# Kernel tuning notes

Hardware: AMD Instinct MI355X
Metric: run time of the kernel (lower is better)

## Reference

```python
import jax, jax.numpy as jnp
import numpy as np

N_NODES = 50000
N_EDGES = 800000
HIDDEN = 128


def setup_inputs() -> dict:
    key = jax.random.key(0)
    k1, k2, k3, k4, k5 = jax.random.split(key, 5)
    x = jax.random.normal(k1, (N_NODES, HIDDEN), dtype=jnp.float32)
    src = jax.random.randint(k2, (N_EDGES,), 0, N_NODES, dtype=jnp.int32)
    # guarantee every node has in-degree >= 1 so deg**-0.5 is finite
    dst = jnp.concatenate([
        jnp.arange(N_NODES, dtype=jnp.int32),
        jax.random.randint(k3, (N_EDGES - N_NODES,), 0, N_NODES, dtype=jnp.int32),
    ])
    edge_index = jnp.stack([src, dst], axis=0)  # [2, E] (row0=j/src, row1=i/dst)
    # nn.Linear(hidden, hidden) params (reused twice in the original module)
    lim = 1.0 / np.sqrt(HIDDEN)
    W = jax.random.uniform(k4, (HIDDEN, HIDDEN), jnp.float32, -lim, lim)
    b = jax.random.uniform(k5, (HIDDEN,), jnp.float32, -lim, lim)
    return {"x": x, "W": W, "b": b, "edge_index": edge_index}


def reference(x, W, b, edge_index):
    src, dst = edge_index[0], edge_index[1]  # (j, i)
    n = x.shape[0]
    # in-degree via scatter-add
    deg = jnp.zeros((n,), x.dtype).at[dst].add(jnp.ones_like(dst, x.dtype))
    deg_inv_sqrt = deg ** -0.5
    norm = deg_inv_sqrt[src] * deg_inv_sqrt[dst]  # [E]
    # first linear (same weights used twice in original)
    h = x @ W.T + b  # [N, H]
    # COO SpMM: gather source rows, scale, scatter-add to destinations
    msg = h[src] * norm[:, None]  # [E, H]
    agg = jax.ops.segment_sum(msg, dst, num_segments=n)  # [N, H]
    # second linear + exact-erf GELU (torch default); dropout is identity in eval
    out = jax.nn.gelu(agg @ W.T + b, approximate=False)
    return out
```

## Files before the change

### kernel.cpp

```cpp
#include <hip/hip_runtime.h>
#include <hip/hip_bf16.h>

#define HIDDEN 128
#define CAP 64
#define BCAP 8192
#define CHUNK 1024

typedef __attribute__((ext_vector_type(8))) short bf16x8;
typedef __attribute__((ext_vector_type(4))) float f32x4;

__device__ __forceinline__ unsigned short f2bf(float f) {
    unsigned int u = __float_as_uint(f);
    u += 0x7FFFu + ((u >> 16) & 1u);
    return (unsigned short)(u >> 16);
}

__device__ __forceinline__ float bflo(unsigned int u) { return __uint_as_float(u << 16); }
__device__ __forceinline__ float bfhi(unsigned int u) { return __uint_as_float(u & 0xffff0000u); }

__global__ void prep_kernel(const float* __restrict__ x, const float* __restrict__ W,
                            unsigned short* __restrict__ xb, unsigned short* __restrict__ wb,
                            int nx4, int nw4, int partBlocks,
                            const int* __restrict__ ei, int E,
                            unsigned int* __restrict__ cursor,
                            unsigned int* __restrict__ lists,
                            int N) {
    __shared__ unsigned int hist[256], basea[256], cur[256];
    if ((int)blockIdx.x >= partBlocks) {
        int i = (blockIdx.x - partBlocks) * blockDim.x + threadIdx.x;
        if (i < nx4) {
            float4 v = ((const float4*)x)[i];
            ushort4 o;
            o.x = f2bf(v.x); o.y = f2bf(v.y); o.z = f2bf(v.z); o.w = f2bf(v.w);
            ((ushort4*)xb)[i] = o;
        } else {
            int j = i - nx4;
            if (j < nw4) {
                float4 v = ((const float4*)W)[j];
                ushort4 o;
                o.x = f2bf(v.x); o.y = f2bf(v.y); o.z = f2bf(v.z); o.w = f2bf(v.w);
                ((ushort4*)wb)[j] = o;
            }
        }
        return;
    }
    int e0 = blockIdx.x * CHUNK;
    int e1 = e0 + CHUNK; if (e1 > E) e1 = E;
    int tid = threadIdx.x;
    hist[tid] = 0;
    __syncthreads();
    for (int e = e0 + tid; e < e1; e += 256)
        atomicAdd(&hist[ei[E + e] >> 8], 1u);
    __syncthreads();
    unsigned int h = hist[tid];
    basea[tid] = h ? atomicAdd(&cursor[tid], h) : 0u;
    cur[tid] = 0;
    __syncthreads();
    for (int e = e0 + tid; e < e1; e += 256) {
        int s = ei[e];
        int d = ei[E + e];
        int bk = d >> 8;
        unsigned int pos = atomicAdd(&cur[bk], 1u) + basea[bk];
        if (pos < BCAP)
            lists[(size_t)bk * BCAP + pos] = ((unsigned int)s << 8) | (unsigned int)(d & 255);
    }
}

__global__ void buildcsr_kernel(const unsigned int* __restrict__ cursor,
                                const unsigned int* __restrict__ lists,
                                unsigned short* __restrict__ csr,
                                unsigned char* __restrict__ cnt_out,
                                float* __restrict__ dinv, int N) {
    __shared__ unsigned int lcnt[256];
    __shared__ unsigned short lcsr[256 * CAP];
    int b = blockIdx.x;
    int tid = threadIdx.x;
    lcnt[tid] = 0;
    __syncthreads();
    int count = (int)cursor[b]; if (count > BCAP) count = BCAP;
    for (int i = tid; i < count; i += 256) {
        unsigned int pk = lists[(size_t)b * BCAP + i];
        int local = pk & 255;
        unsigned int slot = atomicAdd(&lcnt[local], 1u);
        if (slot < CAP) lcsr[local * CAP + slot] = (unsigned short)(pk >> 8);
    }
    __syncthreads();
    int node = b * 256 + tid;
    if (node < N) {
        unsigned int deg = lcnt[tid];
        cnt_out[node] = (unsigned char)(deg > CAP ? CAP : deg);
        dinv[node] = deg ? rsqrtf((float)deg) : 0.0f;
    }
    const unsigned int* s32 = (const unsigned int*)lcsr;
    unsigned int* d32 = (unsigned int*)(csr + (size_t)b * 256 * CAP);
#pragma unroll
    for (int i = 0; i < 256 * CAP / 2 / 256; i++)
        d32[tid + i * 256] = s32[tid + i * 256];
}

__global__ void agg_kernel(const unsigned char* __restrict__ cnt,
                           const unsigned short* __restrict__ csr,
                           const float* __restrict__ dinv,
                           const unsigned short* __restrict__ xb,
                           unsigned short* __restrict__ yb, float* __restrict__ cvec, int n) {
    int lane = threadIdx.x & 63;
    int wid  = threadIdx.x >> 6;
    int gl   = lane & 15;
    int node = blockIdx.x * 16 + wid * 4 + (lane >> 4);
    if (node >= n) return;

    int deg = cnt[node];
    float di = dinv[node];
    const unsigned short* seg = csr + (size_t)node * CAP;

    float acc0 = 0, acc1 = 0, acc2 = 0, acc3 = 0, acc4 = 0, acc5 = 0, acc6 = 0, acc7 = 0;
    float fs = 0.0f;

    for (int be = 0; be < deg; be += 16) {
        int m = deg - be; if (m > 16) m = 16;
        int sv = (gl < m) ? (int)seg[be + gl] : 0;
        float dvv = (gl < m) ? dinv[sv] : 0.0f;
        for (int e = 0; e < m; e++) {
            int s = __shfl(sv, e, 16);
            float f = __shfl(dvv, e, 16) * di;
            fs += f;
            uint4 hv = *(const uint4*)(xb + (size_t)s * HIDDEN + gl * 8);
            acc0 += f * bflo(hv.x); acc1 += f * bfhi(hv.x);
            acc2 += f * bflo(hv.y); acc3 += f * bfhi(hv.y);
            acc4 += f * bflo(hv.z); acc5 += f * bfhi(hv.z);
            acc6 += f * bflo(hv.w); acc7 += f * bfhi(hv.w);
        }
    }

    uint4 o;
    o.x = (unsigned int)f2bf(acc0) | ((unsigned int)f2bf(acc1) << 16);
    o.y = (unsigned int)f2bf(acc2) | ((unsigned int)f2bf(acc3) << 16);
    o.z = (unsigned int)f2bf(acc4) | ((unsigned int)f2bf(acc5) << 16);
    o.w = (unsigned int)f2bf(acc6) | ((unsigned int)f2bf(acc7) << 16);
    *(uint4*)(yb + (size_t)node * HIDDEN + gl * 8) = o;
    if (gl == 0) cvec[node] = fs;
}

__global__ void dgemm_kernel(const unsigned short* __restrict__ yb,
                             const unsigned short* __restrict__ wb,
                             const float* __restrict__ bias,
                             const float* __restrict__ cvec,
                             float* __restrict__ out, int nrows) {
    __shared__ unsigned short wlds[HIDDEN * HIDDEN];
    __shared__ unsigned short zs[4][16][136];
    int lane = threadIdx.x & 63;
    int wave = threadIdx.x >> 6;
    int base = blockIdx.x * 64 + wave * 16;
    int hi = lane >> 4, lo = lane & 15;

    for (int ci = threadIdx.x; ci < 1024; ci += 256) {
        int r = ci >> 3, c32 = ci & 7;
        const uint4* src = (const uint4*)(wb + (size_t)r * HIDDEN + c32 * 16);
        uint4 v0 = src[0], v1 = src[1];
        int b0 = r * 256 + c32 * 32;
        int sw = (r & 7) << 4;
        *(uint4*)((char*)wlds + (b0 ^ sw)) = v0;
        *(uint4*)((char*)wlds + ((b0 + 16) ^ sw)) = v1;
    }

    int arow = base + lo;
    if (arow >= nrows) arow = nrows - 1;
    const bf16x8* Ap = (const bf16x8*)(yb + (size_t)arow * HIDDEN + hi * 8);
    bf16x8 a0 = Ap[0], a1 = Ap[4], a2 = Ap[8], a3 = Ap[12];
    __syncthreads();

#define BFRAG(T, KK) \
    (*(const bf16x8*)((const char*)wlds + \
        ((((T) * 16 + lo) * 256 + (KK) * 64 + hi * 16) ^ ((lo & 7) << 4))))

    f32x4 acc[8];
#pragma unroll
    for (int t = 0; t < 8; t++) acc[t] = (f32x4)(0.0f);
#pragma unroll
    for (int t = 0; t < 8; t++) {
        acc[t] = __builtin_amdgcn_mfma_f32_16x16x32_bf16(a0, BFRAG(t, 0), acc[t], 0, 0, 0);
        acc[t] = __builtin_amdgcn_mfma_f32_16x16x32_bf16(a1, BFRAG(t, 1), acc[t], 0, 0, 0);
        acc[t] = __builtin_amdgcn_mfma_f32_16x16x32_bf16(a2, BFRAG(t, 2), acc[t], 0, 0, 0);
        acc[t] = __builtin_amdgcn_mfma_f32_16x16x32_bf16(a3, BFRAG(t, 3), acc[t], 0, 0, 0);
    }

    float cv[4];
#pragma unroll
    for (int i = 0; i < 4; i++) {
        int r = base + hi * 4 + i;
        cv[i] = cvec[r < nrows ? r : nrows - 1];
    }
#pragma unroll
    for (int t = 0; t < 8; t++) {
        float bv = bias[t * 16 + lo];
#pragma unroll
        for (int i = 0; i < 4; i++)
            zs[wave][hi * 4 + i][t * 16 + lo] = f2bf(acc[t][i] + cv[i] * bv);
    }

    bf16x8 z0 = *(const bf16x8*)&zs[wave][lo][0 * 32 + hi * 8];
    bf16x8 z1 = *(const bf16x8*)&zs[wave][lo][1 * 32 + hi * 8];
    bf16x8 z2 = *(const bf16x8*)&zs[wave][lo][2 * 32 + hi * 8];
    bf16x8 z3 = *(const bf16x8*)&zs[wave][lo][3 * 32 + hi * 8];

    f32x4 acc2[8];
#pragma unroll
    for (int t = 0; t < 8; t++) acc2[t] = (f32x4)(0.0f);
#pragma unroll
    for (int t = 0; t < 8; t++) {
        acc2[t] = __builtin_amdgcn_mfma_f32_16x16x32_bf16(z0, BFRAG(t, 0), acc2[t], 0, 0, 0);
        acc2[t] = __builtin_amdgcn_mfma_f32_16x16x32_bf16(z1, BFRAG(t, 1), acc2[t], 0, 0, 0);
        acc2[t] = __builtin_amdgcn_mfma_f32_16x16x32_bf16(z2, BFRAG(t, 2), acc2[t], 0, 0, 0);
        acc2[t] = __builtin_amdgcn_mfma_f32_16x16x32_bf16(z3, BFRAG(t, 3), acc2[t], 0, 0, 0);
    }
#undef BFRAG

#pragma unroll
    for (int t = 0; t < 8; t++) {
        int col = t * 16 + lo;
        float bv = bias[col];
#pragma unroll
        for (int i = 0; i < 4; i++) {
            int r = base + hi * 4 + i;
            if (r < nrows) {
                float v = acc2[t][i] + bv;
                v = 0.5f * v * (1.0f + erff(v * 0.70710678118f));
                out[(size_t)r * HIDDEN + col] = v;
            }
        }
    }
}

extern "C" void kernel_launch(void* const* d_in, const int* in_sizes, int n_in,
                              void* d_out, int out_size, void* d_ws, size_t ws_size,
                              hipStream_t stream) {
    const float* x  = (const float*)d_in[0];
    const float* W  = (const float*)d_in[1];
    const float* b  = (const float*)d_in[2];
    const int*   ei = (const int*)d_in[3];

    int N = in_sizes[0] / HIDDEN;
    int E = in_sizes[3] / 2;
    int NB = (N + 255) >> 8;

    char* ws = (char*)d_ws;
    size_t off = 0;
    unsigned int* cursor = (unsigned int*)(ws + off);    off += 1024;
    unsigned int* lists = (unsigned int*)(ws + off);     off += (((size_t)NB * BCAP * 4) + 255) & ~255ull;
    unsigned short* csr = (unsigned short*)(ws + off);   off += (((size_t)NB * 256 * CAP * 2) + 255) & ~255ull;
    unsigned char* cnt = (unsigned char*)(ws + off);     off += (((size_t)N) + 255) & ~255ull;
    float* dinv = (float*)(ws + off);                    off += (((size_t)N * 4) + 255) & ~255ull;
    unsigned short* xb = (unsigned short*)(ws + off);    off += (((size_t)N * HIDDEN * 2) + 255) & ~255ull;
    unsigned short* wb = (unsigned short*)(ws + off);    off += ((HIDDEN * HIDDEN * 2) + 255) & ~255ull;
    unsigned short* yb = (unsigned short*)(ws + off);    off += (((size_t)N * HIDDEN * 2) + 255) & ~255ull;
    float* cvec = (float*)(ws + off);                    off += (((size_t)N * 4) + 255) & ~255ull;

    hipMemsetAsync(cursor, 0, 1024, stream);

    int nx4 = N * HIDDEN / 4, nw4 = HIDDEN * HIDDEN / 4;
    int convBlocks = (nx4 + nw4 + 255) / 256;
    int partBlocks = (E + CHUNK - 1) / CHUNK;
    prep_kernel<<<partBlocks + convBlocks, 256, 0, stream>>>(
        x, W, xb, wb, nx4, nw4, partBlocks, ei, E, cursor, lists, N);
    buildcsr_kernel<<<NB, 256, 0, stream>>>(cursor, lists, csr, cnt, dinv, N);
    agg_kernel<<<(N + 15) / 16, 256, 0, stream>>>(cnt, csr, dinv, xb, yb, cvec, N);
    dgemm_kernel<<<(N + 63) / 64, 256, 0, stream>>>(yb, wb, b, cvec, (float*)d_out, N);
}
```

Baseline: 167.8 us.

## Fuse sparse aggregation into the dense double-GEMM kernel via LDS staging

Merges the gather-based aggregation kernel into the MFMA GEMM kernel. Each wave now aggregates its own 16 rows, four nodes at a time, into shared memory, then feeds them straight into the two chained matmuls. This removes the global write and re-read of the intermediate bf16 matrix and the cvec array, plus one kernel launch. In exchange each block does more serial work before the MFMA phase, and the grid is 4x smaller (64 nodes per block instead of 16), which may reduce latency hiding for the irregular gathers. The 32KB of weights in LDS also limits occupancy for the gather phase.

```diff
diff --git a/kernel.cpp b/kernel.cpp
--- a/kernel.cpp
+++ b/kernel.cpp
@@ -98,56 +98,16 @@
         d32[tid + i * 256] = s32[tid + i * 256];
 }
 
-__global__ void agg_kernel(const unsigned char* __restrict__ cnt,
-                           const unsigned short* __restrict__ csr,
-                           const float* __restrict__ dinv,
-                           const unsigned short* __restrict__ xb,
-                           unsigned short* __restrict__ yb, float* __restrict__ cvec, int n) {
-    int lane = threadIdx.x & 63;
-    int wid  = threadIdx.x >> 6;
-    int gl   = lane & 15;
-    int node = blockIdx.x * 16 + wid * 4 + (lane >> 4);
-    if (node >= n) return;
-
-    int deg = cnt[node];
-    float di = dinv[node];
-    const unsigned short* seg = csr + (size_t)node * CAP;
-
-    float acc0 = 0, acc1 = 0, acc2 = 0, acc3 = 0, acc4 = 0, acc5 = 0, acc6 = 0, acc7 = 0;
-    float fs = 0.0f;
-
-    for (int be = 0; be < deg; be += 16) {
-        int m = deg - be; if (m > 16) m = 16;
-        int sv = (gl < m) ? (int)seg[be + gl] : 0;
-        float dvv = (gl < m) ? dinv[sv] : 0.0f;
-        for (int e = 0; e < m; e++) {
-            int s = __shfl(sv, e, 16);
-            float f = __shfl(dvv, e, 16) * di;
-            fs += f;
-            uint4 hv = *(const uint4*)(xb + (size_t)s * HIDDEN + gl * 8);
-            acc0 += f * bflo(hv.x); acc1 += f * bfhi(hv.x);
-            acc2 += f * bflo(hv.y); acc3 += f * bfhi(hv.y);
-            acc4 += f * bflo(hv.z); acc5 += f * bfhi(hv.z);
-            acc6 += f * bflo(hv.w); acc7 += f * bfhi(hv.w);
-        }
-    }
-
-    uint4 o;
-    o.x = (unsigned int)f2bf(acc0) | ((unsigned int)f2bf(acc1) << 16);
-    o.y = (unsigned int)f2bf(acc2) | ((unsigned int)f2bf(acc3) << 16);
-    o.z = (unsigned int)f2bf(acc4) | ((unsigned int)f2bf(acc5) << 16);
-    o.w = (unsigned int)f2bf(acc6) | ((unsigned int)f2bf(acc7) << 16);
-    *(uint4*)(yb + (size_t)node * HIDDEN + gl * 8) = o;
-    if (gl == 0) cvec[node] = fs;
-}
-
-__global__ void dgemm_kernel(const unsigned short* __restrict__ yb,
-                             const unsigned short* __restrict__ wb,
-                             const float* __restrict__ bias,
-                             const float* __restrict__ cvec,
-                             float* __restrict__ out, int nrows) {
+__global__ void aggdgemm_kernel(const unsigned char* __restrict__ cnt,
+                                const unsigned short* __restrict__ csr,
+                                const float* __restrict__ dinv,
+                                const unsigned short* __restrict__ xb,
+                                const unsigned short* __restrict__ wb,
+                                const float* __restrict__ bias,
+                                float* __restrict__ out, int nrows) {
     __shared__ unsigned short wlds[HIDDEN * HIDDEN];
-    __shared__ unsigned short zs[4][16][136];
+    __shared__ unsigned short ys[4][16][136];
+    __shared__ float cfs[4][16];
     int lane = threadIdx.x & 63;
     int wave = threadIdx.x >> 6;
     int base = blockIdx.x * 64 + wave * 16;
@@ -163,15 +123,48 @@
         *(uint4*)((char*)wlds + ((b0 + 16) ^ sw)) = v1;
     }
 
-    int arow = base + lo;
-    if (arow >= nrows) arow = nrows - 1;
-    const bf16x8* Ap = (const bf16x8*)(yb + (size_t)arow * HIDDEN + hi * 8);
-    bf16x8 a0 = Ap[0], a1 = Ap[4], a2 = Ap[8], a3 = Ap[12];
+    for (int nb = 0; nb < 4; nb++) {
+        int node = base + nb * 4 + hi;
+        int deg = 0;
+        float di = 0.0f;
+        if (node < nrows) { deg = cnt[node]; di = dinv[node]; }
+        const unsigned short* seg = csr + (size_t)node * CAP;
+
+        float a0 = 0, a1 = 0, a2 = 0, a3 = 0, a4 = 0, a5 = 0, a6 = 0, a7 = 0;
+        float fs = 0.0f;
+        for (int be = 0; be < deg; be += 16) {
+            int m = deg - be; if (m > 16) m = 16;
+            int sv = (lo < m) ? (int)seg[be + lo] : 0;
+            float dvv = (lo < m) ? dinv[sv] : 0.0f;
+            for (int e = 0; e < m; e++) {
+                int s = __shfl(sv, e, 16);
+                float f = __shfl(dvv, e, 16) * di;
+                fs += f;
+                uint4 hv = *(const uint4*)(xb + (size_t)s * HIDDEN + lo * 8);
+                a0 += f * bflo(hv.x); a1 += f * bfhi(hv.x);
+                a2 += f * bflo(hv.y); a3 += f * bfhi(hv.y);
+                a4 += f * bflo(hv.z); a5 += f * bfhi(hv.z);
+                a6 += f * bflo(hv.w); a7 += f * bfhi(hv.w);
+            }
+        }
+        uint4 o;
+        o.x = (unsigned int)f2bf(a0) | ((unsigned int)f2bf(a1) << 16);
+        o.y = (unsigned int)f2bf(a2) | ((unsigned int)f2bf(a3) << 16);
+        o.z = (unsigned int)f2bf(a4) | ((unsigned int)f2bf(a5) << 16);
+        o.w = (unsigned int)f2bf(a6) | ((unsigned int)f2bf(a7) << 16);
+        *(uint4*)&ys[wave][nb * 4 + hi][lo * 8] = o;
+        if (lo == 0) cfs[wave][nb * 4 + hi] = fs;
+    }
     __syncthreads();
 
 #define BFRAG(T, KK) \
     (*(const bf16x8*)((const char*)wlds + \
         ((((T) * 16 + lo) * 256 + (KK) * 64 + hi * 16) ^ ((lo & 7) << 4))))
+
+    bf16x8 a0 = *(const bf16x8*)&ys[wave][lo][0 * 32 + hi * 8];
+    bf16x8 a1 = *(const bf16x8*)&ys[wave][lo][1 * 32 + hi * 8];
+    bf16x8 a2 = *(const bf16x8*)&ys[wave][lo][2 * 32 + hi * 8];
+    bf16x8 a3 = *(const bf16x8*)&ys[wave][lo][3 * 32 + hi * 8];
 
     f32x4 acc[8];
 #pragma unroll
@@ -186,22 +179,19 @@
 
     float cv[4];
 #pragma unroll
-    for (int i = 0; i < 4; i++) {
-        int r = base + hi * 4 + i;
-        cv[i] = cvec[r < nrows ? r : nrows - 1];
-    }
+    for (int i = 0; i < 4; i++) cv[i] = cfs[wave][hi * 4 + i];
 #pragma unroll
     for (int t = 0; t < 8; t++) {
         float bv = bias[t * 16 + lo];
 #pragma unroll
         for (int i = 0; i < 4; i++)
-            zs[wave][hi * 4 + i][t * 16 + lo] = f2bf(acc[t][i] + cv[i] * bv);
-    }
-
-    bf16x8 z0 = *(const bf16x8*)&zs[wave][lo][0 * 32 + hi * 8];
-    bf16x8 z1 = *(const bf16x8*)&zs[wave][lo][1 * 32 + hi * 8];
-    bf16x8 z2 = *(const bf16x8*)&zs[wave][lo][2 * 32 + hi * 8];
-    bf16x8 z3 = *(const bf16x8*)&zs[wave][lo][3 * 32 + hi * 8];
+            ys[wave][hi * 4 + i][t * 16 + lo] = f2bf(acc[t][i] + cv[i] * bv);
+    }
+
+    bf16x8 z0 = *(const bf16x8*)&ys[wave][lo][0 * 32 + hi * 8];
+    bf16x8 z1 = *(const bf16x8*)&ys[wave][lo][1 * 32 + hi * 8];
+    bf16x8 z2 = *(const bf16x8*)&ys[wave][lo][2 * 32 + hi * 8];
+    bf16x8 z3 = *(const bf16x8*)&ys[wave][lo][3 * 32 + hi * 8];
 
     f32x4 acc2[8];
 #pragma unroll
@@ -252,8 +242,6 @@
     float* dinv = (float*)(ws + off);                    off += (((size_t)N * 4) + 255) & ~255ull;
     unsigned short* xb = (unsigned short*)(ws + off);    off += (((size_t)N * HIDDEN * 2) + 255) & ~255ull;
     unsigned short* wb = (unsigned short*)(ws + off);    off += ((HIDDEN * HIDDEN * 2) + 255) & ~255ull;
-    unsigned short* yb = (unsigned short*)(ws + off);    off += (((size_t)N * HIDDEN * 2) + 255) & ~255ull;
-    float* cvec = (float*)(ws + off);                    off += (((size_t)N * 4) + 255) & ~255ull;
 
     hipMemsetAsync(cursor, 0, 1024, stream);
 
@@ -263,6 +251,6 @@
     prep_kernel<<<partBlocks + convBlocks, 256, 0, stream>>>(
         x, W, xb, wb, nx4, nw4, partBlocks, ei, E, cursor, lists, N);
     buildcsr_kernel<<<NB, 256, 0, stream>>>(cursor, lists, csr, cnt, dinv, N);
-    agg_kernel<<<(N + 15) / 16, 256, 0, stream>>>(cnt, csr, dinv, xb, yb, cvec, N);
-    dgemm_kernel<<<(N + 63) / 64, 256, 0, stream>>>(yb, wb, b, cvec, (float*)d_out, N);
-}
+    aggdgemm_kernel<<<(N + 63) / 64, 256, 0, stream>>>(cnt, csr, dinv, xb, wb, b,
+                                                       (float*)d_out, N);
+}
```

New measurement: 207.1 us. 23.4% more time.

## Split bf16 feature matrix into column slices to shrink gather working set

Applied to the files above, without the earlier changes.

Stores the bf16 copy of x as four 32-column slices, each laid out contiguously over all nodes. The aggregation kernel now processes one slice per block (interleaved by blockIdx), so each gathered row is 64 bytes and the set of rows touched by concurrently running blocks fits better in cache. The GEMM reads the sliced aggregate and is widened to 512 threads handling 128 rows per block. The cost is that the CSR segment and dinv values are read four times, and each gather is a narrower 8-byte load per lane.

```diff
diff --git a/kernel.cpp b/kernel.cpp
--- a/kernel.cpp
+++ b/kernel.cpp
@@ -5,6 +5,7 @@
 #define CAP 64
 #define BCAP 8192
 #define CHUNK 1024
+#define SCOLS 32
 
 typedef __attribute__((ext_vector_type(8))) short bf16x8;
 typedef __attribute__((ext_vector_type(4))) float f32x4;
@@ -19,7 +20,7 @@
 __device__ __forceinline__ float bfhi(unsigned int u) { return __uint_as_float(u & 0xffff0000u); }
 
 __global__ void prep_kernel(const float* __restrict__ x, const float* __restrict__ W,
-                            unsigned short* __restrict__ xb, unsigned short* __restrict__ wb,
+                            unsigned short* __restrict__ xbs, unsigned short* __restrict__ wb,
                             int nx4, int nw4, int partBlocks,
                             const int* __restrict__ ei, int E,
                             unsigned int* __restrict__ cursor,
@@ -32,7 +33,8 @@
             float4 v = ((const float4*)x)[i];
             ushort4 o;
             o.x = f2bf(v.x); o.y = f2bf(v.y); o.z = f2bf(v.z); o.w = f2bf(v.w);
-            ((ushort4*)xb)[i] = o;
+            int row = i >> 5, q = i & 31;
+            *(ushort4*)(xbs + ((size_t)(q >> 3) * N + row) * SCOLS + (q & 7) * 4) = o;
         } else {
             int j = i - nx4;
             if (j < nw4) {
@@ -101,59 +103,57 @@
 __global__ void agg_kernel(const unsigned char* __restrict__ cnt,
                            const unsigned short* __restrict__ csr,
                            const float* __restrict__ dinv,
-                           const unsigned short* __restrict__ xb,
-                           unsigned short* __restrict__ yb, float* __restrict__ cvec, int n) {
+                           const unsigned short* __restrict__ xbs,
+                           unsigned short* __restrict__ ybs, float* __restrict__ cvec, int n) {
+    int slice = blockIdx.x & 3;
+    int chunk = blockIdx.x >> 2;
     int lane = threadIdx.x & 63;
-    int wid  = threadIdx.x >> 6;
-    int gl   = lane & 15;
-    int node = blockIdx.x * 16 + wid * 4 + (lane >> 4);
+    int wave = threadIdx.x >> 6;
+    int g  = lane >> 3;
+    int gl = lane & 7;
+    int node = chunk * 32 + wave * 8 + g;
     if (node >= n) return;
 
     int deg = cnt[node];
     float di = dinv[node];
     const unsigned short* seg = csr + (size_t)node * CAP;
-
-    float acc0 = 0, acc1 = 0, acc2 = 0, acc3 = 0, acc4 = 0, acc5 = 0, acc6 = 0, acc7 = 0;
+    const unsigned short* xs  = xbs + (size_t)slice * n * SCOLS;
+
+    float a0 = 0, a1 = 0, a2 = 0, a3 = 0;
     float fs = 0.0f;
-
-    for (int be = 0; be < deg; be += 16) {
-        int m = deg - be; if (m > 16) m = 16;
+    for (int be = 0; be < deg; be += 8) {
+        int m = deg - be; if (m > 8) m = 8;
         int sv = (gl < m) ? (int)seg[be + gl] : 0;
         float dvv = (gl < m) ? dinv[sv] : 0.0f;
         for (int e = 0; e < m; e++) {
-            int s = __shfl(sv, e, 16);
-            float f = __shfl(dvv, e, 16) * di;
+            int s = __shfl(sv, e, 8);
+            float f = __shfl(dvv, e, 8) * di;
             fs += f;
-            uint4 hv = *(const uint4*)(xb + (size_t)s * HIDDEN + gl * 8);
-            acc0 += f * bflo(hv.x); acc1 += f * bfhi(hv.x);
-            acc2 += f * bflo(hv.y); acc3 += f * bfhi(hv.y);
-            acc4 += f * bflo(hv.z); acc5 += f * bfhi(hv.z);
-            acc6 += f * bflo(hv.w); acc7 += f * bfhi(hv.w);
+            uint2 hv = *(const uint2*)(xs + (size_t)s * SCOLS + gl * 4);
+            a0 += f * bflo(hv.x); a1 += f * bfhi(hv.x);
+            a2 += f * bflo(hv.y); a3 += f * bfhi(hv.y);
         }
     }
-
-    uint4 o;
-    o.x = (unsigned int)f2bf(acc0) | ((unsigned int)f2bf(acc1) << 16);
-    o.y = (unsigned int)f2bf(acc2) | ((unsigned int)f2bf(acc3) << 16);
-    o.z = (unsigned int)f2bf(acc4) | ((unsigned int)f2bf(acc5) << 16);
-    o.w = (unsigned int)f2bf(acc6) | ((unsigned int)f2bf(acc7) << 16);
-    *(uint4*)(yb + (size_t)node * HIDDEN + gl * 8) = o;
-    if (gl == 0) cvec[node] = fs;
-}
-
-__global__ void dgemm_kernel(const unsigned short* __restrict__ yb,
+    uint2 o;
+    o.x = (unsigned int)f2bf(a0) | ((unsigned int)f2bf(a1) << 16);
+    o.y = (unsigned int)f2bf(a2) | ((unsigned int)f2bf(a3) << 16);
+    *(uint2*)(ybs + ((size_t)slice * n + node) * SCOLS + gl * 4) = o;
+    if (slice == 0 && gl == 0) cvec[node] = fs;
+}
+
+__global__ void dgemm_kernel(const unsigned short* __restrict__ ybs,
                              const unsigned short* __restrict__ wb,
                              const float* __restrict__ bias,
                              const float* __restrict__ cvec,
                              float* __restrict__ out, int nrows) {
     __shared__ unsigned short wlds[HIDDEN * HIDDEN];
-    __shared__ unsigned short zs[4][16][136];
+    __shared__ unsigned short zs[8][16][136];
     int lane = threadIdx.x & 63;
     int wave = threadIdx.x >> 6;
-    int base = blockIdx.x * 64 + wave * 16;
+    int base = blockIdx.x * 128 + wave * 16;
     int hi = lane >> 4, lo = lane & 15;
 
-    for (int ci = threadIdx.x; ci < 1024; ci += 256) {
+    for (int ci = threadIdx.x; ci < 1024; ci += 512) {
         int r = ci >> 3, c32 = ci & 7;
         const uint4* src = (const uint4*)(wb + (size_t)r * HIDDEN + c32 * 16);
         uint4 v0 = src[0], v1 = src[1];
@@ -165,8 +165,10 @@
 
     int arow = base + lo;
     if (arow >= nrows) arow = nrows - 1;
-    const bf16x8* Ap = (const bf16x8*)(yb + (size_t)arow * HIDDEN + hi * 8);
-    bf16x8 a0 = Ap[0], a1 = Ap[4], a2 = Ap[8], a3 = Ap[12];
+    bf16x8 a0 = *(const bf16x8*)(ybs + ((size_t)0 * nrows + arow) * SCOLS + hi * 8);
+    bf16x8 a1 = *(const bf16x8*)(ybs + ((size_t)1 * nrows + arow) * SCOLS + hi * 8);
+    bf16x8 a2 = *(const bf16x8*)(ybs + ((size_t)2 * nrows + arow) * SCOLS + hi * 8);
+    bf16x8 a3 = *(const bf16x8*)(ybs + ((size_t)3 * nrows + arow) * SCOLS + hi * 8);
     __syncthreads();
 
 #define BFRAG(T, KK) \
@@ -250,9 +252,9 @@
     unsigned short* csr = (unsigned short*)(ws + off);   off += (((size_t)NB * 256 * CAP * 2) + 255) & ~255ull;
     unsigned char* cnt = (unsigned char*)(ws + off);     off += (((size_t)N) + 255) & ~255ull;
     float* dinv = (float*)(ws + off);                    off += (((size_t)N * 4) + 255) & ~255ull;
-    unsigned short* xb = (unsigned short*)(ws + off);    off += (((size_t)N * HIDDEN * 2) + 255) & ~255ull;
+    unsigned short* xbs = (unsigned short*)(ws + off);   off += (((size_t)N * HIDDEN * 2) + 255) & ~255ull;
     unsigned short* wb = (unsigned short*)(ws + off);    off += ((HIDDEN * HIDDEN * 2) + 255) & ~255ull;
-    unsigned short* yb = (unsigned short*)(ws + off);    off += (((size_t)N * HIDDEN * 2) + 255) & ~255ull;
+    unsigned short* ybs = (unsigned short*)(ws + off);   off += (((size_t)N * HIDDEN * 2) + 255) & ~255ull;
     float* cvec = (float*)(ws + off);                    off += (((size_t)N * 4) + 255) & ~255ull;
 
     hipMemsetAsync(cursor, 0, 1024, stream);
@@ -261,8 +263,9 @@
     int convBlocks = (nx4 + nw4 + 255) / 256;
     int partBlocks = (E + CHUNK - 1) / CHUNK;
     prep_kernel<<<partBlocks + convBlocks, 256, 0, stream>>>(
-        x, W, xb, wb, nx4, nw4, partBlocks, ei, E, cursor, lists, N);
+        x, W, xbs, wb, nx4, nw4, partBlocks, ei, E, cursor, lists, N);
     buildcsr_kernel<<<NB, 256, 0, stream>>>(cursor, lists, csr, cnt, dinv, N);
-    agg_kernel<<<(N + 15) / 16, 256, 0, stream>>>(cnt, csr, dinv, xb, yb, cvec, N);
-    dgemm_kernel<<<(N + 63) / 64, 256, 0, stream>>>(yb, wb, b, cvec, (float*)d_out, N);
-}
+    int chunks = (N + 31) / 32;
+    agg_kernel<<<chunks * 4, 256, 0, stream>>>(cnt, csr, dinv, xbs, ybs, cvec, N);
+    dgemm_kernel<<<(N + 127) / 128, 512, 0, stream>>>(ybs, wb, b, cvec, (float*)d_out, N);
+}
```

After: 176.8 us. 5.3% more time.

## Replace global-atomic bucket partition with per-chunk local sort and offsets; widen GEMM blocks

Applied to the files above, without the earlier changes.

The edge partition step now sorts each 1024-edge chunk by destination bucket in shared memory and writes the chunk with per-bucket prefix offsets. Global cursor atomics and the memset are no longer needed. The CSR builder reads the matching segment from every chunk instead of one contiguous bucket list, which turns contiguous reads into many small strided ones across roughly 782 chunks per block. The dense GEMM moves to 512-thread blocks covering 128 rows each, so the weight tile loaded into LDS is shared by more rows.

```diff
diff --git a/kernel.cpp b/kernel.cpp
--- a/kernel.cpp
+++ b/kernel.cpp
@@ -3,8 +3,8 @@
 
 #define HIDDEN 128
 #define CAP 64
-#define BCAP 8192
 #define CHUNK 1024
+#define LOFS_STRIDE 200
 
 typedef __attribute__((ext_vector_type(8))) short bf16x8;
 typedef __attribute__((ext_vector_type(4))) float f32x4;
@@ -22,10 +22,11 @@
                             unsigned short* __restrict__ xb, unsigned short* __restrict__ wb,
                             int nx4, int nw4, int partBlocks,
                             const int* __restrict__ ei, int E,
-                            unsigned int* __restrict__ cursor,
-                            unsigned int* __restrict__ lists,
-                            int N) {
-    __shared__ unsigned int hist[256], basea[256], cur[256];
+                            unsigned int* __restrict__ lists2,
+                            int* __restrict__ lofs,
+                            int NBK) {
+    __shared__ unsigned int hist[256], cur[256];
+    __shared__ unsigned int lsorted[CHUNK];
     if ((int)blockIdx.x >= partBlocks) {
         int i = (blockIdx.x - partBlocks) * blockDim.x + threadIdx.x;
         if (i < nx4) {
@@ -44,45 +45,67 @@
         }
         return;
     }
-    int e0 = blockIdx.x * CHUNK;
+    int blk = blockIdx.x;
+    int e0 = blk * CHUNK;
     int e1 = e0 + CHUNK; if (e1 > E) e1 = E;
     int tid = threadIdx.x;
+
+    int es[4], ed[4];
+#pragma unroll
+    for (int k = 0; k < 4; k++) {
+        int e = e0 + tid + k * 256;
+        if (e < e1) { es[k] = ei[e]; ed[k] = ei[E + e]; }
+        else        { es[k] = 0;     ed[k] = -1; }
+    }
     hist[tid] = 0;
     __syncthreads();
-    for (int e = e0 + tid; e < e1; e += 256)
-        atomicAdd(&hist[ei[E + e] >> 8], 1u);
-    __syncthreads();
-    unsigned int h = hist[tid];
-    basea[tid] = h ? atomicAdd(&cursor[tid], h) : 0u;
+#pragma unroll
+    for (int k = 0; k < 4; k++)
+        if (ed[k] >= 0) atomicAdd(&hist[ed[k] >> 8], 1u);
+    __syncthreads();
+    for (int o = 1; o < 256; o <<= 1) {
+        unsigned int u = (tid >= o) ? hist[tid - o] : 0u;
+        __syncthreads();
+        hist[tid] += u;
+        __syncthreads();
+    }
+    if (tid <= NBK) lofs[blk * LOFS_STRIDE + tid] = tid ? (int)hist[tid - 1] : 0;
     cur[tid] = 0;
     __syncthreads();
-    for (int e = e0 + tid; e < e1; e += 256) {
-        int s = ei[e];
-        int d = ei[E + e];
-        int bk = d >> 8;
-        unsigned int pos = atomicAdd(&cur[bk], 1u) + basea[bk];
-        if (pos < BCAP)
-            lists[(size_t)bk * BCAP + pos] = ((unsigned int)s << 8) | (unsigned int)(d & 255);
-    }
-}
-
-__global__ void buildcsr_kernel(const unsigned int* __restrict__ cursor,
-                                const unsigned int* __restrict__ lists,
+#pragma unroll
+    for (int k = 0; k < 4; k++)
+        if (ed[k] >= 0) {
+            int bk = ed[k] >> 8;
+            unsigned int p = (bk ? hist[bk - 1] : 0u) + atomicAdd(&cur[bk], 1u);
+            lsorted[p] = ((unsigned int)es[k] << 8) | (unsigned int)(ed[k] & 255);
+        }
+    __syncthreads();
+#pragma unroll
+    for (int k = 0; k < 4; k++)
+        lists2[(size_t)blk * CHUNK + tid + k * 256] = lsorted[tid + k * 256];
+}
+
+__global__ void buildcsr_kernel(const unsigned int* __restrict__ lists2,
+                                const int* __restrict__ lofs,
                                 unsigned short* __restrict__ csr,
                                 unsigned char* __restrict__ cnt_out,
-                                float* __restrict__ dinv, int N) {
+                                float* __restrict__ dinv, int N, int partBlocks) {
     __shared__ unsigned int lcnt[256];
     __shared__ unsigned short lcsr[256 * CAP];
     int b = blockIdx.x;
     int tid = threadIdx.x;
     lcnt[tid] = 0;
     __syncthreads();
-    int count = (int)cursor[b]; if (count > BCAP) count = BCAP;
-    for (int i = tid; i < count; i += 256) {
-        unsigned int pk = lists[(size_t)b * BCAP + i];
-        int local = pk & 255;
-        unsigned int slot = atomicAdd(&lcnt[local], 1u);
-        if (slot < CAP) lcsr[local * CAP + slot] = (unsigned short)(pk >> 8);
+    for (int sb = tid; sb < partBlocks; sb += 256) {
+        int s0 = lofs[sb * LOFS_STRIDE + b];
+        int s1 = lofs[sb * LOFS_STRIDE + b + 1];
+        const unsigned int* lp = lists2 + (size_t)sb * CHUNK;
+        for (int i = s0; i < s1; i++) {
+            unsigned int pk = lp[i];
+            int local = pk & 255;
+            unsigned int slot = atomicAdd(&lcnt[local], 1u);
+            if (slot < CAP) lcsr[local * CAP + slot] = (unsigned short)(pk >> 8);
+        }
     }
     __syncthreads();
     int node = b * 256 + tid;
@@ -113,7 +136,7 @@
     float di = dinv[node];
     const unsigned short* seg = csr + (size_t)node * CAP;
 
-    float acc0 = 0, acc1 = 0, acc2 = 0, acc3 = 0, acc4 = 0, acc5 = 0, acc6 = 0, acc7 = 0;
+    float a0 = 0, a1 = 0, a2 = 0, a3 = 0, a4 = 0, a5 = 0, a6 = 0, a7 = 0;
     float fs = 0.0f;
 
     for (int be = 0; be < deg; be += 16) {
@@ -125,18 +148,18 @@
             float f = __shfl(dvv, e, 16) * di;
             fs += f;
             uint4 hv = *(const uint4*)(xb + (size_t)s * HIDDEN + gl * 8);
-            acc0 += f * bflo(hv.x); acc1 += f * bfhi(hv.x);
-            acc2 += f * bflo(hv.y); acc3 += f * bfhi(hv.y);
-            acc4 += f * bflo(hv.z); acc5 += f * bfhi(hv.z);
-            acc6 += f * bflo(hv.w); acc7 += f * bfhi(hv.w);
+            a0 += f * bflo(hv.x); a1 += f * bfhi(hv.x);
+            a2 += f * bflo(hv.y); a3 += f * bfhi(hv.y);
+            a4 += f * bflo(hv.z); a5 += f * bfhi(hv.z);
+            a6 += f * bflo(hv.w); a7 += f * bfhi(hv.w);
         }
     }
 
     uint4 o;
-    o.x = (unsigned int)f2bf(acc0) | ((unsigned int)f2bf(acc1) << 16);
-    o.y = (unsigned int)f2bf(acc2) | ((unsigned int)f2bf(acc3) << 16);
-    o.z = (unsigned int)f2bf(acc4) | ((unsigned int)f2bf(acc5) << 16);
-    o.w = (unsigned int)f2bf(acc6) | ((unsigned int)f2bf(acc7) << 16);
+    o.x = (unsigned int)f2bf(a0) | ((unsigned int)f2bf(a1) << 16);
+    o.y = (unsigned int)f2bf(a2) | ((unsigned int)f2bf(a3) << 16);
+    o.z = (unsigned int)f2bf(a4) | ((unsigned int)f2bf(a5) << 16);
+    o.w = (unsigned int)f2bf(a6) | ((unsigned int)f2bf(a7) << 16);
     *(uint4*)(yb + (size_t)node * HIDDEN + gl * 8) = o;
     if (gl == 0) cvec[node] = fs;
 }
@@ -147,13 +170,13 @@
                              const float* __restrict__ cvec,
                              float* __restrict__ out, int nrows) {
     __shared__ unsigned short wlds[HIDDEN * HIDDEN];
-    __shared__ unsigned short zs[4][16][136];
+    __shared__ unsigned short zs[8][16][136];
     int lane = threadIdx.x & 63;
     int wave = threadIdx.x >> 6;
-    int base = blockIdx.x * 64 + wave * 16;
+    int base = blockIdx.x * 128 + wave * 16;
     int hi = lane >> 4, lo = lane & 15;
 
-    for (int ci = threadIdx.x; ci < 1024; ci += 256) {
+    for (int ci = threadIdx.x; ci < 1024; ci += 512) {
         int r = ci >> 3, c32 = ci & 7;
         const uint4* src = (const uint4*)(wb + (size_t)r * HIDDEN + c32 * 16);
         uint4 v0 = src[0], v1 = src[1];
@@ -242,27 +265,25 @@
     int N = in_sizes[0] / HIDDEN;
     int E = in_sizes[3] / 2;
     int NB = (N + 255) >> 8;
+    int partBlocks = (E + CHUNK - 1) / CHUNK;
 
     char* ws = (char*)d_ws;
     size_t off = 0;
-    unsigned int* cursor = (unsigned int*)(ws + off);    off += 1024;
-    unsigned int* lists = (unsigned int*)(ws + off);     off += (((size_t)NB * BCAP * 4) + 255) & ~255ull;
-    unsigned short* csr = (unsigned short*)(ws + off);   off += (((size_t)NB * 256 * CAP * 2) + 255) & ~255ull;
-    unsigned char* cnt = (unsigned char*)(ws + off);     off += (((size_t)N) + 255) & ~255ull;
-    float* dinv = (float*)(ws + off);                    off += (((size_t)N * 4) + 255) & ~255ull;
-    unsigned short* xb = (unsigned short*)(ws + off);    off += (((size_t)N * HIDDEN * 2) + 255) & ~255ull;
-    unsigned short* wb = (unsigned short*)(ws + off);    off += ((HIDDEN * HIDDEN * 2) + 255) & ~255ull;
-    unsigned short* yb = (unsigned short*)(ws + off);    off += (((size_t)N * HIDDEN * 2) + 255) & ~255ull;
-    float* cvec = (float*)(ws + off);                    off += (((size_t)N * 4) + 255) & ~255ull;
-
-    hipMemsetAsync(cursor, 0, 1024, stream);
+    unsigned int* lists2 = (unsigned int*)(ws + off);   off += (((size_t)partBlocks * CHUNK * 4) + 255) & ~255ull;
+    int* lofs = (int*)(ws + off);                       off += (((size_t)partBlocks * LOFS_STRIDE * 4) + 255) & ~255ull;
+    unsigned short* csr = (unsigned short*)(ws + off);  off += (((size_t)NB * 256 * CAP * 2) + 255) & ~255ull;
+    unsigned char* cnt = (unsigned char*)(ws + off);    off += (((size_t)NB * 256) + 255) & ~255ull;
+    float* dinv = (float*)(ws + off);                   off += (((size_t)N * 4) + 255) & ~255ull;
+    unsigned short* xb = (unsigned short*)(ws + off);   off += (((size_t)N * HIDDEN * 2) + 255) & ~255ull;
+    unsigned short* wb = (unsigned short*)(ws + off);   off += ((HIDDEN * HIDDEN * 2) + 255) & ~255ull;
+    unsigned short* yb = (unsigned short*)(ws + off);   off += (((size_t)N * HIDDEN * 2) + 255) & ~255ull;
+    float* cvec = (float*)(ws + off);                   off += (((size_t)N * 4) + 255) & ~255ull;
 
     int nx4 = N * HIDDEN / 4, nw4 = HIDDEN * HIDDEN / 4;
     int convBlocks = (nx4 + nw4 + 255) / 256;
-    int partBlocks = (E + CHUNK - 1) / CHUNK;
     prep_kernel<<<partBlocks + convBlocks, 256, 0, stream>>>(
-        x, W, xb, wb, nx4, nw4, partBlocks, ei, E, cursor, lists, N);
-    buildcsr_kernel<<<NB, 256, 0, stream>>>(cursor, lists, csr, cnt, dinv, N);
+        x, W, xb, wb, nx4, nw4, partBlocks, ei, E, lists2, lofs, NB);
+    buildcsr_kernel<<<NB, 256, 0, stream>>>(lists2, lofs, csr, cnt, dinv, N, partBlocks);
     agg_kernel<<<(N + 15) / 16, 256, 0, stream>>>(cnt, csr, dinv, xb, yb, cvec, N);
-    dgemm_kernel<<<(N + 63) / 64, 256, 0, stream>>>(yb, wb, b, cvec, (float*)d_out, N);
-}
+    dgemm_kernel<<<(N + 127) / 128, 512, 0, stream>>>(yb, wb, b, cvec, (float*)d_out, N);
+}
```

Measured after the change: 186.1 us. +10.8%, slower.
